# Performance work log

Hardware: AMD Instinct MI355X
Metric: run time of the kernel (lower is better)

Reference implementation:

```python
import jax, jax.numpy as jnp
import numpy as np

EPS_BN = 1e-5


def _square_distance(a, b):
    # a: [B,N,3], b: [B,S,3] -> [B,N,S]
    return (jnp.sum(a * a, -1)[:, :, None]
            - 2.0 * jnp.einsum('bnc,bsc->bns', a, b)
            + jnp.sum(b * b, -1)[:, None, :])


def _bn_relu(x, gamma, beta):
    # x: [B,C,N]; training-mode batch norm over (B,N) per channel
    mean = jnp.mean(x, axis=(0, 2), keepdims=True)
    var = jnp.var(x, axis=(0, 2), keepdims=True)
    y = (x - mean) * jax.lax.rsqrt(var + EPS_BN)
    y = y * gamma[None, :, None] + beta[None, :, None]
    return jax.nn.relu(y)


def setup_inputs() -> dict:
    key = jax.random.key(0)
    ks = jax.random.split(key, 8)
    B, N, S, D1, D2 = 16, 4096, 1024, 128, 256
    Cin, C0, C1 = D1 + D2, 256, 128
    inp = {
        'xyz1': jax.random.normal(ks[0], (B, 3, N), jnp.float32),
        'xyz2': jax.random.normal(ks[1], (B, 3, S), jnp.float32),
        'points1': jax.random.normal(ks[2], (B, D1, N), jnp.float32),
        'points2': jax.random.normal(ks[3], (B, D2, S), jnp.float32),
        # pointwise Conv1d weights (kernel size 1) as [out,in]
        'w0': jax.random.normal(ks[4], (C0, Cin), jnp.float32) * (1.0 / np.sqrt(Cin)),
        'b0': jnp.zeros((C0,), jnp.float32),
        'g0': jnp.ones((C0,), jnp.float32),
        'be0': jnp.zeros((C0,), jnp.float32),
        'w1': jax.random.normal(ks[5], (C1, C0), jnp.float32) * (1.0 / np.sqrt(C0)),
        'b1': jnp.zeros((C1,), jnp.float32),
        'g1': jnp.ones((C1,), jnp.float32),
        'be1': jnp.zeros((C1,), jnp.float32),
    }
    return inp


def reference(xyz1, xyz2, points1, points2, w0, b0, g0, be0, w1, b1, g1, be1):
    # permute to [B,N,3] / [B,S,3] / [B,S,D2]
    x1 = jnp.transpose(xyz1, (0, 2, 1))
    x2 = jnp.transpose(xyz2, (0, 2, 1))
    p2 = jnp.transpose(points2, (0, 2, 1))
    B, N, _ = x1.shape

    dists = _square_distance(x1, x2)            # [B,N,S]
    # NOTE: faithful to the source: idx comes from the sort, but the
    # weight distances are the FIRST 3 columns of the UNsorted dists
    # (the repo assigns sorted values to `dicts`, not `dists`).
    idx = jnp.argsort(dists, axis=-1)[:, :, :3]  # [B,N,3]
    d3 = jnp.maximum(dists[:, :, :3], 1e-10)     # [B,N,3]
    weight = 1.0 / d3
    weight = weight / jnp.sum(weight, axis=-1, keepdims=True)

    gathered = jax.vmap(lambda p, i: p[i])(p2, idx)          # [B,N,3,D2]
    interpolated = jnp.sum(gathered * weight[..., None], axis=2)  # [B,N,D2]

    p1 = jnp.transpose(points1, (0, 2, 1))       # [B,N,D1]
    new_points = jnp.concatenate([p1, interpolated], axis=-1)  # [B,N,Cin]
    new_points = jnp.transpose(new_points, (0, 2, 1))           # [B,Cin,N]

    h = jnp.einsum('oc,bcn->bon', w0, new_points) + b0[None, :, None]
    h = _bn_relu(h, g0, be0)
    h = jnp.einsum('oc,bcn->bon', w1, h) + b1[None, :, None]
    h = _bn_relu(h, g1, be1)
    return h
```

## Files before the change

kernel.cpp:

```cpp
#include <hip/hip_runtime.h>
#include <cstdint>
#include <cstddef>

#define BB   16
#define NN   4096
#define SS   1024
#define D1   128
#define D2   256
#define CIN  384
#define C0   256
#define C1   128
#define MM   (BB*NN)
#define NBLK (MM/128)

typedef __attribute__((ext_vector_type(8))) short short8;
typedef __attribute__((ext_vector_type(4))) float f32x4;

__device__ __forceinline__ float b2f(unsigned short h) {
    union { unsigned int u; float f; } x; x.u = ((unsigned int)h) << 16; return x.f;
}
__device__ __forceinline__ unsigned short f2b(float f) {
    union { float f; unsigned int u; } x; x.f = f;
    unsigned int r = x.u + 0x7FFFu + ((x.u >> 16) & 1u);
    return (unsigned short)(r >> 16);
}

#define GLD16(g, l) __builtin_amdgcn_global_load_lds( \
    (const __attribute__((address_space(1))) void*)(g), \
    (__attribute__((address_space(3))) void*)(l), 16, 0, 0)


#define UPD6(dd, ss, D0, D1v, D2v, J0, J1, J2) do { \
    bool ca = (dd) < D0, cb = (dd) < D1v, cc = (dd) < D2v; \
    float m1 = __builtin_amdgcn_fmed3f((dd), D0, D1v); \
    float m2 = __builtin_amdgcn_fmed3f((dd), D1v, D2v); \
    int u1 = ca ? J0 : (ss); \
    int u2 = cb ? J1 : (ss); \
    D0 = fminf((dd), D0); \
    J2 = cc ? u2 : J2; \
    J1 = cb ? u1 : J1; \
    J0 = ca ? (ss) : J0; \
    D1v = m1; D2v = m2; \
} while (0)

#define LTE(x, xj, y, yj) ((x) < (y) || ((x) == (y) && (xj) < (yj)))

__device__ __forceinline__ void knn_body(const float* __restrict__ xyz1,
                                         const float* __restrict__ xyz2,
                                         int* __restrict__ idxb, float* __restrict__ wtb,
                                         int rb, int t, char* smem)
{
    float* sx = (float*)smem;
    float* sy = sx + 8 * 132;
    float* sz = sy + 8 * 132;
    const int b = rb >> 7;
    const int bx = rb & 127;
    const int chunk = t & 7;
    const int n = bx * 32 + (t >> 3);

    for (int i = t; i < SS; i += 256) {
        int li = (i >> 7) * 132 + (i & 127);
        sx[li] = xyz2[((size_t)b * 3 + 0) * SS + i];
        sy[li] = xyz2[((size_t)b * 3 + 1) * SS + i];
        sz[li] = xyz2[((size_t)b * 3 + 2) * SS + i];
    }
    __syncthreads();

    const float px = xyz1[((size_t)b * 3 + 0) * NN + n];
    const float py = xyz1[((size_t)b * 3 + 1) * NN + n];
    const float pz = xyz1[((size_t)b * 3 + 2) * NN + n];

    float aD0 = 3.4e38f, aD1 = 3.4e38f, aD2 = 3.4e38f;
    int   aJ0 = 0, aJ1 = 0, aJ2 = 0;
    float bD0 = 3.4e38f, bD1 = 3.4e38f, bD2 = 3.4e38f;
    int   bJ0 = 0, bJ1 = 0, bJ2 = 0;

    const float* cx = sx + chunk * 132;
    const float* cy = sy + chunk * 132;
    const float* cz = sz + chunk * 132;
    const int sbase = chunk * 128;
#pragma unroll 4
    for (int s4 = 0; s4 < 32; ++s4) {
        float4 xs = *(const float4*)(cx + s4 * 4);
        float4 ys = *(const float4*)(cy + s4 * 4);
        float4 zs = *(const float4*)(cz + s4 * 4);
        int s = sbase + s4 * 4;
        { float dx=px-xs.x, dy=py-ys.x, dz=pz-zs.x; float d=dx*dx+dy*dy+dz*dz; UPD6(d, s+0, aD0,aD1,aD2,aJ0,aJ1,aJ2); }
        { float dx=px-xs.y, dy=py-ys.y, dz=pz-zs.y; float d=dx*dx+dy*dy+dz*dz; UPD6(d, s+1, bD0,bD1,bD2,bJ0,bJ1,bJ2); }
        { float dx=px-xs.z, dy=py-ys.z, dz=pz-zs.z; float d=dx*dx+dy*dy+dz*dz; UPD6(d, s+2, aD0,aD1,aD2,aJ0,aJ1,aJ2); }
        { float dx=px-xs.w, dy=py-ys.w, dz=pz-zs.w; float d=dx*dx+dy*dy+dz*dz; UPD6(d, s+3, bD0,bD1,bD2,bJ0,bJ1,bJ2); }
    }

    float d0v, d1v, d2v; int j0, j1, j2;
    {
        bool c0 = LTE(aD0, aJ0, bD0, bJ0);
        d0v = c0 ? aD0 : bD0;  j0 = c0 ? aJ0 : bJ0;
        float na0 = c0 ? aD1 : aD0, na1 = c0 ? aD2 : aD1;
        int   nx0 = c0 ? aJ1 : aJ0, nx1 = c0 ? aJ2 : aJ1;
        float nb0 = c0 ? bD0 : bD1, nb1 = c0 ? bD1 : bD2;
        int   ny0 = c0 ? bJ0 : bJ1, ny1 = c0 ? bJ1 : bJ2;
        bool c1 = LTE(na0, nx0, nb0, ny0);
        d1v = c1 ? na0 : nb0;  j1 = c1 ? nx0 : ny0;
        float ma0 = c1 ? na1 : na0;  int mx0 = c1 ? nx1 : nx0;
        float mb0 = c1 ? nb0 : nb1;  int my0 = c1 ? ny0 : ny1;
        bool c2 = LTE(ma0, mx0, mb0, my0);
        d2v = c2 ? ma0 : mb0;  j2 = c2 ? mx0 : my0;
    }

#pragma unroll
    for (int r = 1; r <= 4; r <<= 1) {
        float e0 = __shfl_xor(d0v, r), e1 = __shfl_xor(d1v, r), e2 = __shfl_xor(d2v, r);
        int   k0 = __shfl_xor(j0, r),  k1 = __shfl_xor(j1, r),  k2 = __shfl_xor(j2, r);
        bool ownlow = ((t & r) == 0);
        float a0 = ownlow ? d0v : e0, a1 = ownlow ? d1v : e1, a2 = ownlow ? d2v : e2;
        int   x0 = ownlow ? j0 : k0,  x1 = ownlow ? j1 : k1,  x2 = ownlow ? j2 : k2;
        float b0 = ownlow ? e0 : d0v, b1 = ownlow ? e1 : d1v, b2 = ownlow ? e2 : d2v;
        int   y0 = ownlow ? k0 : j0,  y1 = ownlow ? k1 : j1,  y2 = ownlow ? k2 : j2;
        bool c0 = a0 <= b0;
        d0v = c0 ? a0 : b0;  j0 = c0 ? x0 : y0;
        float na0 = c0 ? a1 : a0, na1 = c0 ? a2 : a1;
        int   nx0 = c0 ? x1 : x0, nx1 = c0 ? x2 : x1;
        float nb0 = c0 ? b0 : b1, nb1 = c0 ? b1 : b2;
        int   ny0 = c0 ? y0 : y1, ny1 = c0 ? y1 : y2;
        bool c1 = na0 <= nb0;
        d1v = c1 ? na0 : nb0;  j1 = c1 ? nx0 : ny0;
        float ma0 = c1 ? na1 : na0;  int mx0 = c1 ? nx1 : nx0;
        float mb0 = c1 ? nb0 : nb1;  int my0 = c1 ? ny0 : ny1;
        bool c2 = ma0 <= mb0;
        d2v = c2 ? ma0 : mb0;  j2 = c2 ? mx0 : my0;
    }

    if (chunk == 0) {
        float dd[3];
#pragma unroll
        for (int k = 0; k < 3; ++k) {
            float dx = px - sx[k], dy = py - sy[k], dz = pz - sz[k];
            float d = dx*dx + dy*dy + dz*dz;
            dd[k] = fmaxf(d, 1e-10f);
        }
        float r0 = 1.f/dd[0], r1 = 1.f/dd[1], r2 = 1.f/dd[2];
        float inv = 1.f / (r0 + r1 + r2);
        size_t base = ((size_t)b * NN + n) * 3;
        idxb[base+0] = j0; idxb[base+1] = j1; idxb[base+2] = j2;
        wtb[base+0] = r0*inv; wtb[base+1] = r1*inv; wtb[base+2] = r2*inv;
    }
}

__device__ __forceinline__ void transpose_body(const float* __restrict__ src,
                                               unsigned short* __restrict__ dst,
                                               int C, int Np, int dstStride,
                                               int b, int cblk, int nblk, int t, char* smem)
{
    float (*tile)[65] = (float(*)[65])smem;
    const int c0 = cblk * 64, n0 = nblk * 64;
    const int j = t & 63, i4 = t >> 6;
#pragma unroll
    for (int p = 0; p < 64; p += 4) {
        int ci = p + i4;
        tile[ci][j] = src[((size_t)b * C + c0 + ci) * Np + n0 + j];
    }
    __syncthreads();
#pragma unroll
    for (int p = 0; p < 64; p += 4) {
        int ni = p + i4;
        dst[((size_t)b * Np + n0 + ni) * dstStride + c0 + j] = f2b(tile[j][ni]);
    }
}

__global__ __launch_bounds__(256) void mega_front_k(
    const float* __restrict__ xyz1, const float* __restrict__ xyz2,
    const float* __restrict__ points1, const float* __restrict__ points2,
    const float* __restrict__ w0, const float* __restrict__ w1,
    unsigned short* __restrict__ P1T, unsigned short* __restrict__ P2T,
    unsigned short* __restrict__ w0b, unsigned short* __restrict__ w1b,
    int* __restrict__ idxb, float* __restrict__ wtb)
{
    __shared__ __align__(16) char smem[16640];
    const unsigned bid = blockIdx.x;
    const int g = bid / 86, r = bid % 86;
    const int t = threadIdx.x;

    if (r < 32) {
        knn_body(xyz1, xyz2, idxb, wtb, g * 32 + r, t, smem);
    } else if (r < 64) {
        int rb = g * 32 + (r - 32);
        transpose_body(points1, P1T, D1, NN, D1,
                       rb >> 7, (rb >> 6) & 1, rb & 63, t, smem);
    } else if (r < 80) {
        int rb = g * 16 + (r - 64);
        transpose_body(points2, P2T, D2, SS, D2,
                       rb >> 6, (rb >> 4) & 3, rb & 15, t, smem);
    } else {
        int rb = g * 6 + (r - 80);
        int i = rb * 256 + t;
        if (i < C0 * CIN) w0b[i] = f2b(w0[i]);
        if (i < C1 * C0)  w1b[i] = f2b(w1[i]);
    }
}

__launch_bounds__(512, 1)
__global__ void gemm1_k(const unsigned short* __restrict__ P1T,
                        const unsigned short* __restrict__ P2T,
                        const int* __restrict__ idxb, const float* __restrict__ wtb,
                        const unsigned short* __restrict__ w0b,
                        unsigned short* __restrict__ h1, float* __restrict__ part1)
{
    __shared__ unsigned short Als[128 * 64];
    __shared__ unsigned short Bls[256 * 64];
    __shared__ float lsum[2][256];
    __shared__ float lsq[2][256];

    const int t = threadIdx.x;
    const int wv = t >> 6, l = t & 63, g = l >> 4, lc = l & 15;
    const int wm = wv >> 2, wn = wv & 3;
    const int m0 = blockIdx.x * 128;
    const int b  = blockIdx.x >> 5;
    const int sub = t & 7;

    const int grow = t >> 2;
    const size_t gb = ((size_t)(m0 + grow)) * 3;
    const int gi0 = idxb[gb], gi1 = idxb[gb+1], gi2 = idxb[gb+2];
    const float gw0 = wtb[gb], gw1 = wtb[gb+1], gw2 = wtb[gb+2];
    const char* gp0 = (const char*)(P2T + ((size_t)b * SS + gi0) * D2) + (t & 3) * 32;
    const char* gp1 = (const char*)(P2T + ((size_t)b * SS + gi1) * D2) + (t & 3) * 32;
    const char* gp2 = (const char*)(P2T + ((size_t)b * SS + gi2) * D2) + (t & 3) * 32;
    char* gdst = (char*)Als + grow * 128;
    const int gsw = (grow & 7) << 4;

    f32x4 acc[4][4];
#pragma unroll
    for (int i = 0; i < 4; ++i)
#pragma unroll
        for (int j = 0; j < 4; ++j) acc[i][j] = (f32x4){0.f, 0.f, 0.f, 0.f};

    for (int ks = 0; ks < 6; ++ks) {
        const int k0 = ks * 64;
        __syncthreads();
        if (ks < 2) {
#pragma unroll
            for (int q = 0; q < 2; ++q) {
                int row = q * 64 + (t >> 3);
                int bco = (sub * 16) ^ ((row & 7) << 4);
                const char* src = (const char*)P1T + (((size_t)(m0 + row)) * D1 + k0) * 2 + bco;
                char* dst = (char*)Als + (q * 512 + wv * 64) * 16;
                GLD16(src, dst);
            }
        } else {
            const int cgB = (ks - 2) * 128;
#pragma unroll
            for (int h = 0; h < 2; ++h) {
                union { uint4 v; unsigned short s[8]; } a0, a1, a2, ov;
                a0.v = *(const uint4*)(gp0 + cgB + h * 16);
                a1.v = *(const uint4*)(gp1 + cgB + h * 16);
                a2.v = *(const uint4*)(gp2 + cgB + h * 16);
#pragma unroll
                for (int i = 0; i < 8; ++i)
                    ov.s[i] = f2b(gw0 * b2f(a0.s[i]) + gw1 * b2f(a1.s[i]) + gw2 * b2f(a2.s[i]));
                *(uint4*)(gdst + (((t & 3) * 32 + h * 16) ^ gsw)) = ov.v;
            }
        }
#pragma unroll
        for (int q = 0; q < 4; ++q) {
            int o = q * 64 + (t >> 3);
            int bco = (sub * 16) ^ ((o & 7) << 4);
            const char* src = (const char*)w0b + (((size_t)o) * CIN + k0) * 2 + bco;
            char* dst = (char*)Bls + (q * 512 + wv * 64) * 16;
            GLD16(src, dst);
        }
        __syncthreads();
#pragma unroll
        for (int kk = 0; kk < 2; ++kk) {
            short8 af[4], bfr[4];
#pragma unroll
            for (int fm = 0; fm < 4; ++fm) {
                int row = wm * 64 + fm * 16 + lc;
                int bcol = kk * 64 + g * 16;
                af[fm] = *(const short8*)((const char*)Als + row * 128 + (bcol ^ ((row & 7) << 4)));
            }
#pragma unroll
            for (int fn = 0; fn < 4; ++fn) {
                int o = wn * 64 + fn * 16 + lc;
                int bcol = kk * 64 + g * 16;
                bfr[fn] = *(const short8*)((const char*)Bls + o * 128 + (bcol ^ ((o & 7) << 4)));
            }
#pragma unroll
            for (int fm = 0; fm < 4; ++fm)
#pragma unroll
                for (int fn = 0; fn < 4; ++fn)
                    acc[fm][fn] = __builtin_amdgcn_mfma_f32_16x16x32_bf16(af[fm], bfr[fn], acc[fm][fn], 0, 0, 0);
        }
    }

    float s1[4] = {0,0,0,0}, s2v[4] = {0,0,0,0};
#pragma unroll
    for (int fm = 0; fm < 4; ++fm)
#pragma unroll
        for (int fn = 0; fn < 4; ++fn) {
            int row = m0 + wm * 64 + fm * 16 + g * 4;
            int col = wn * 64 + fn * 16 + lc;
#pragma unroll
            for (int j = 0; j < 4; ++j) {
                float v = acc[fm][fn][j];
                h1[((size_t)(row + j)) * C0 + col] = f2b(v);
                s1[fn] += v; s2v[fn] += v * v;
            }
        }
#pragma unroll
    for (int fn = 0; fn < 4; ++fn) {
        s1[fn] += __shfl_xor(s1[fn], 16); s1[fn] += __shfl_xor(s1[fn], 32);
        s2v[fn] += __shfl_xor(s2v[fn], 16); s2v[fn] += __shfl_xor(s2v[fn], 32);
    }
    if (l < 16) {
#pragma unroll
        for (int fn = 0; fn < 4; ++fn) {
            lsum[wm][wn * 64 + fn * 16 + l] = s1[fn];
            lsq[wm][wn * 64 + fn * 16 + l] = s2v[fn];
        }
    }
    __syncthreads();
    if (t < 256) {
        part1[(size_t)t * NBLK + blockIdx.x]        = lsum[0][t] + lsum[1][t];
        part1[(size_t)(C0 + t) * NBLK + blockIdx.x] = lsq[0][t] + lsq[1][t];
    }
}

__global__ void stats_k(const float* __restrict__ part, int nblk, int C,
                        const float* __restrict__ gam, const float* __restrict__ bet,
                        float* __restrict__ sc, float* __restrict__ sh)
{
    const int w = threadIdx.x >> 6, l = threadIdx.x & 63;
    const int o = blockIdx.x * 4 + w;
    if (o >= C) return;
    float s = 0.f, q = 0.f;
    for (int i = l; i < nblk; i += 64) {
        s += part[(size_t)o * nblk + i];
        q += part[(size_t)(C + o) * nblk + i];
    }
#pragma unroll
    for (int r = 32; r; r >>= 1) { s += __shfl_xor(s, r); q += __shfl_xor(q, r); }
    if (l == 0) {
        const float inv = 1.0f / (float)MM;
        float mean = s * inv;
        float var = q * inv - mean * mean;
        float scale = gam[o] * rsqrtf(var + 1e-5f);
        sc[o] = scale;
        sh[o] = bet[o] - mean * scale;
    }
}

__launch_bounds__(256, 1)
__global__ void gemm2_k(const unsigned short* __restrict__ h1, const unsigned short* __restrict__ w1b,
                        const float* __restrict__ sc1, const float* __restrict__ sh1,
                        unsigned short* __restrict__ h2, float* __restrict__ part2)
{
    __shared__ unsigned short Als[128 * 64];
    __shared__ unsigned short Bls[128 * 64];
    __shared__ float scl[256], shl[256];
    __shared__ float lsum[2][128];
    __shared__ float lsq[2][128];

    const int t = threadIdx.x;
    const int wv = t >> 6, l = t & 63, g = l >> 4, lc = l & 15;
    const int wm = wv >> 1, wn = wv & 1;
    const int m0 = blockIdx.x * 128;
    const int sub = t & 7;

    scl[t] = sc1[t]; shl[t] = sh1[t];

    f32x4 acc[4][4];
#pragma unroll
    for (int i = 0; i < 4; ++i)
#pragma unroll
        for (int j = 0; j < 4; ++j) acc[i][j] = (f32x4){0.f, 0.f, 0.f, 0.f};

    for (int ks = 0; ks < 4; ++ks) {
        const int k0 = ks * 64;
        __syncthreads();
        uint4 r[4];
#pragma unroll
        for (int q = 0; q < 4; ++q) {
            int row = q * 32 + (t >> 3);
            r[q] = *(const uint4*)((const char*)h1 + (((size_t)(m0 + row)) * C0 + k0) * 2 + sub * 16);
        }
#pragma unroll
        for (int q = 0; q < 4; ++q) {
            int row = q * 32 + (t >> 3);
            union { uint4 v; unsigned short s[8]; } u, ov;
            u.v = r[q];
#pragma unroll
            for (int i = 0; i < 8; ++i) {
                int k = k0 + sub * 8 + i;
                float f = b2f(u.s[i]);
                ov.s[i] = f2b(fmaxf(0.0f, fmaf(scl[k], f, shl[k])));
            }
            *(uint4*)((char*)Als + row * 128 + ((sub * 16) ^ ((row & 7) << 4))) = ov.v;
        }
#pragma unroll
        for (int q = 0; q < 4; ++q) {
            int o = q * 32 + (t >> 3);
            int bco = (sub * 16) ^ ((o & 7) << 4);
            const char* src = (const char*)w1b + (((size_t)o) * C0 + k0) * 2 + bco;
            char* dst = (char*)Bls + (q * 256 + wv * 64) * 16;
            GLD16(src, dst);
        }
        __syncthreads();
#pragma unroll
        for (int kk = 0; kk < 2; ++kk) {
            short8 af[4], bfr[4];
#pragma unroll
            for (int fm = 0; fm < 4; ++fm) {
                int row = wm * 64 + fm * 16 + lc;
                int bcol = kk * 64 + g * 16;
                af[fm] = *(const short8*)((const char*)Als + row * 128 + (bcol ^ ((row & 7) << 4)));
            }
#pragma unroll
            for (int fn = 0; fn < 4; ++fn) {
                int o = wn * 64 + fn * 16 + lc;
                int bcol = kk * 64 + g * 16;
                bfr[fn] = *(const short8*)((const char*)Bls + o * 128 + (bcol ^ ((o & 7) << 4)));
            }
#pragma unroll
            for (int fm = 0; fm < 4; ++fm)
#pragma unroll
                for (int fn = 0; fn < 4; ++fn)
                    acc[fm][fn] = __builtin_amdgcn_mfma_f32_16x16x32_bf16(af[fm], bfr[fn], acc[fm][fn], 0, 0, 0);
        }
    }

    float s1[4] = {0,0,0,0}, s2v[4] = {0,0,0,0};
#pragma unroll
    for (int fm = 0; fm < 4; ++fm)
#pragma unroll
        for (int fn = 0; fn < 4; ++fn) {
            int row = m0 + wm * 64 + fm * 16 + g * 4;
            int col = wn * 64 + fn * 16 + lc;
#pragma unroll
            for (int j = 0; j < 4; ++j) {
                float v = acc[fm][fn][j];
                h2[((size_t)(row + j)) * C1 + col] = f2b(v);
                s1[fn] += v; s2v[fn] += v * v;
            }
        }
#pragma unroll
    for (int fn = 0; fn < 4; ++fn) {
        s1[fn] += __shfl_xor(s1[fn], 16); s1[fn] += __shfl_xor(s1[fn], 32);
        s2v[fn] += __shfl_xor(s2v[fn], 16); s2v[fn] += __shfl_xor(s2v[fn], 32);
    }
    if (l < 16) {
#pragma unroll
        for (int fn = 0; fn < 4; ++fn) {
            lsum[wm][wn * 64 + fn * 16 + l] = s1[fn];
            lsq[wm][wn * 64 + fn * 16 + l] = s2v[fn];
        }
    }
    __syncthreads();
    if (t < 128) {
        part2[(size_t)t * NBLK + blockIdx.x]        = lsum[0][t] + lsum[1][t];
        part2[(size_t)(C1 + t) * NBLK + blockIdx.x] = lsq[0][t] + lsq[1][t];
    }
}

__global__ void finalize_k(const unsigned short* __restrict__ h2,
                           const float* __restrict__ sc, const float* __restrict__ sh,
                           float* __restrict__ out)
{
    __shared__ float tile[64][65];
    const int b = blockIdx.z, o0 = blockIdx.y * 64, n0 = blockIdx.x * 64;
    const int t = threadIdx.x, j = t & 63, i4 = t >> 6;
    const float scv = sc[o0 + j], shv = sh[o0 + j];
#pragma unroll
    for (int p = 0; p < 64; p += 4) {
        int ni = p + i4;
        float f = b2f(h2[((size_t)b * NN + n0 + ni) * C1 + o0 + j]);
        tile[ni][j] = fmaxf(0.0f, fmaf(scv, f, shv));
    }
    __syncthreads();
#pragma unroll
    for (int p = 0; p < 64; p += 4) {
        int oi = p + i4;
        out[((size_t)(b * C1 + o0 + oi)) * NN + n0 + j] = tile[j][oi];
    }
}

extern "C" void kernel_launch(void* const* d_in, const int* in_sizes, int n_in,
                              void* d_out, int out_size, void* d_ws, size_t ws_size,
                              hipStream_t stream)
{
    const float* xyz1    = (const float*)d_in[0];
    const float* xyz2    = (const float*)d_in[1];
    const float* points1 = (const float*)d_in[2];
    const float* points2 = (const float*)d_in[3];
    const float* w0      = (const float*)d_in[4];
    const float* g0      = (const float*)d_in[6];
    const float* be0     = (const float*)d_in[7];
    const float* w1      = (const float*)d_in[8];
    const float* g1      = (const float*)d_in[10];
    const float* be1     = (const float*)d_in[11];
    float* out = (float*)d_out;
    char* ws = (char*)d_ws;

    unsigned short* P1T = (unsigned short*)(ws + 0);
    unsigned short* h1  = (unsigned short*)(ws + 16777216);
    unsigned short* P2T = (unsigned short*)(ws + 50331648);
    unsigned short* h2  = (unsigned short*)(ws + 58720256);
    int*   idxb  = (int*)  (ws + 75497472);
    float* wtb   = (float*)(ws + 76283904);
    unsigned short* w0b = (unsigned short*)(ws + 77070336);
    unsigned short* w1b = (unsigned short*)(ws + 77266944);
    float* part1 = (float*)(ws + 77332480);
    float* part2 = (float*)(ws + 78381056);
    float* sc1   = (float*)(ws + 78905344);
    float* sh1   = (float*)(ws + 78906368);
    float* sc2   = (float*)(ws + 78907392);
    float* sh2   = (float*)(ws + 78908416);

    mega_front_k<<<86 * 64, 256, 0, stream>>>(xyz1, xyz2, points1, points2, w0, w1,
                                              P1T, P2T, w0b, w1b, idxb, wtb);
    gemm1_k<<<MM/128, 512, 0, stream>>>(P1T, P2T, idxb, wtb, w0b, h1, part1);
    stats_k<<<C0/4, 256, 0, stream>>>(part1, NBLK, C0, g0, be0, sc1, sh1);
    gemm2_k<<<MM/128, 256, 0, stream>>>(h1, w1b, sc1, sh1, h2, part2);
    stats_k<<<C1/4, 256, 0, stream>>>(part2, NBLK, C1, g1, be1, sc2, sh2);
    finalize_k<<<dim3(NN/64, C1/64, BB), 256, 0, stream>>>(h2, sc2, sh2, out);
}
```

Before: 117.4 us.

## Rewrite KNN top-3 with packed double keys and wave-split merge

Replaces the KNN top-3 selection with packed 64-bit keys (float distance in the high word, index in the low word), so min/max on doubles keep distance and index together and a sorting network replaces the compare/select chains. Each block now handles 64 query points with four waves, each scanning a quarter of the candidates straight from global memory, then merges through LDS. This drops the xyz2 LDS staging and the shuffle reduction, and halves the KNN block count, so the mega-kernel grid shrinks. The risk is FP64 min/max throughput and uncached-looking global loads replacing LDS reads. Tie-breaking by index is kept implicitly.

```diff
diff --git a/kernel.cpp b/kernel.cpp
--- a/kernel.cpp
+++ b/kernel.cpp
@@ -29,116 +29,88 @@
     (const __attribute__((address_space(1))) void*)(g), \
     (__attribute__((address_space(3))) void*)(l), 16, 0, 0)
 
-
-#define UPD6(dd, ss, D0, D1v, D2v, J0, J1, J2) do { \
-    bool ca = (dd) < D0, cb = (dd) < D1v, cc = (dd) < D2v; \
-    float m1 = __builtin_amdgcn_fmed3f((dd), D0, D1v); \
-    float m2 = __builtin_amdgcn_fmed3f((dd), D1v, D2v); \
-    int u1 = ca ? J0 : (ss); \
-    int u2 = cb ? J1 : (ss); \
-    D0 = fminf((dd), D0); \
-    J2 = cc ? u2 : J2; \
-    J1 = cb ? u1 : J1; \
-    J0 = ca ? (ss) : J0; \
-    D1v = m1; D2v = m2; \
-} while (0)
-
-#define LTE(x, xj, y, yj) ((x) < (y) || ((x) == (y) && (xj) < (yj)))
-
-__device__ __forceinline__ void knn_body(const float* __restrict__ xyz1,
-                                         const float* __restrict__ xyz2,
-                                         int* __restrict__ idxb, float* __restrict__ wtb,
-                                         int rb, int t, char* smem)
-{
-    float* sx = (float*)smem;
-    float* sy = sx + 8 * 132;
-    float* sz = sy + 8 * 132;
-    const int b = rb >> 7;
-    const int bx = rb & 127;
-    const int chunk = t & 7;
-    const int n = bx * 32 + (t >> 3);
-
-    for (int i = t; i < SS; i += 256) {
-        int li = (i >> 7) * 132 + (i & 127);
-        sx[li] = xyz2[((size_t)b * 3 + 0) * SS + i];
-        sy[li] = xyz2[((size_t)b * 3 + 1) * SS + i];
-        sz[li] = xyz2[((size_t)b * 3 + 2) * SS + i];
-    }
-    __syncthreads();
+__device__ __forceinline__ void knn_body3(const float* __restrict__ xyz1,
+                                          const float* __restrict__ xyz2,
+                                          int* __restrict__ idxb, float* __restrict__ wtb,
+                                          int rb, int t, char* smem)
+{
+    double* mrg = (double*)smem;
+    const int b    = rb >> 6;
+    const int lane = t & 63;
+    const int n    = (rb & 63) * 64 + lane;
+    const int wu   = __builtin_amdgcn_readfirstlane(t >> 6);
+
+    const float* qx = xyz2 + ((size_t)b * 3 + 0) * SS + wu * 256;
+    const float* qy = xyz2 + ((size_t)b * 3 + 1) * SS + wu * 256;
+    const float* qz = xyz2 + ((size_t)b * 3 + 2) * SS + wu * 256;
 
     const float px = xyz1[((size_t)b * 3 + 0) * NN + n];
     const float py = xyz1[((size_t)b * 3 + 1) * NN + n];
     const float pz = xyz1[((size_t)b * 3 + 2) * NN + n];
 
-    float aD0 = 3.4e38f, aD1 = 3.4e38f, aD2 = 3.4e38f;
-    int   aJ0 = 0, aJ1 = 0, aJ2 = 0;
-    float bD0 = 3.4e38f, bD1 = 3.4e38f, bD2 = 3.4e38f;
-    int   bJ0 = 0, bJ1 = 0, bJ2 = 0;
-
-    const float* cx = sx + chunk * 132;
-    const float* cy = sy + chunk * 132;
-    const float* cz = sz + chunk * 132;
-    const int sbase = chunk * 128;
+    const double INITK = __hiloint2double(0x7F7FFFFF, 0);
+    double A0 = INITK, A1 = INITK, A2 = INITK;
+    double B0 = INITK, B1 = INITK, B2 = INITK;
+    const int sb = wu * 256;
+
 #pragma unroll 4
-    for (int s4 = 0; s4 < 32; ++s4) {
-        float4 xs = *(const float4*)(cx + s4 * 4);
-        float4 ys = *(const float4*)(cy + s4 * 4);
-        float4 zs = *(const float4*)(cz + s4 * 4);
-        int s = sbase + s4 * 4;
-        { float dx=px-xs.x, dy=py-ys.x, dz=pz-zs.x; float d=dx*dx+dy*dy+dz*dz; UPD6(d, s+0, aD0,aD1,aD2,aJ0,aJ1,aJ2); }
-        { float dx=px-xs.y, dy=py-ys.y, dz=pz-zs.y; float d=dx*dx+dy*dy+dz*dz; UPD6(d, s+1, bD0,bD1,bD2,bJ0,bJ1,bJ2); }
-        { float dx=px-xs.z, dy=py-ys.z, dz=pz-zs.z; float d=dx*dx+dy*dy+dz*dz; UPD6(d, s+2, aD0,aD1,aD2,aJ0,aJ1,aJ2); }
-        { float dx=px-xs.w, dy=py-ys.w, dz=pz-zs.w; float d=dx*dx+dy*dy+dz*dz; UPD6(d, s+3, bD0,bD1,bD2,bJ0,bJ1,bJ2); }
-    }
-
-    float d0v, d1v, d2v; int j0, j1, j2;
+    for (int s = 0; s < 256; s += 2) {
+        {
+            float qxv = qx[s], qyv = qy[s], qzv = qz[s];
+            float dx = px - qxv, dy = py - qyv, dz = pz - qzv;
+            float d = dx*dx + dy*dy + dz*dz;
+            double k = __hiloint2double(__float_as_int(d), sb + s);
+            double t0 = fmin(k, A0), h0 = fmax(k, A0);
+            double t1 = fmin(h0, A1), h1 = fmax(h0, A1);
+            A2 = fmin(h1, A2); A0 = t0; A1 = t1;
+        }
+        {
+            float qxv = qx[s+1], qyv = qy[s+1], qzv = qz[s+1];
+            float dx = px - qxv, dy = py - qyv, dz = pz - qzv;
+            float d = dx*dx + dy*dy + dz*dz;
+            double k = __hiloint2double(__float_as_int(d), sb + s + 1);
+            double t0 = fmin(k, B0), h0 = fmax(k, B0);
+            double t1 = fmin(h0, B1), h1 = fmax(h0, B1);
+            B2 = fmin(h1, B2); B0 = t0; B1 = t1;
+        }
+    }
+    double K0, K1, K2;
     {
-        bool c0 = LTE(aD0, aJ0, bD0, bJ0);
-        d0v = c0 ? aD0 : bD0;  j0 = c0 ? aJ0 : bJ0;
-        float na0 = c0 ? aD1 : aD0, na1 = c0 ? aD2 : aD1;
-        int   nx0 = c0 ? aJ1 : aJ0, nx1 = c0 ? aJ2 : aJ1;
-        float nb0 = c0 ? bD0 : bD1, nb1 = c0 ? bD1 : bD2;
-        int   ny0 = c0 ? bJ0 : bJ1, ny1 = c0 ? bJ1 : bJ2;
-        bool c1 = LTE(na0, nx0, nb0, ny0);
-        d1v = c1 ? na0 : nb0;  j1 = c1 ? nx0 : ny0;
-        float ma0 = c1 ? na1 : na0;  int mx0 = c1 ? nx1 : nx0;
-        float mb0 = c1 ? nb0 : nb1;  int my0 = c1 ? ny0 : ny1;
-        bool c2 = LTE(ma0, mx0, mb0, my0);
-        d2v = c2 ? ma0 : mb0;  j2 = c2 ? mx0 : my0;
-    }
-
-#pragma unroll
-    for (int r = 1; r <= 4; r <<= 1) {
-        float e0 = __shfl_xor(d0v, r), e1 = __shfl_xor(d1v, r), e2 = __shfl_xor(d2v, r);
-        int   k0 = __shfl_xor(j0, r),  k1 = __shfl_xor(j1, r),  k2 = __shfl_xor(j2, r);
-        bool ownlow = ((t & r) == 0);
-        float a0 = ownlow ? d0v : e0, a1 = ownlow ? d1v : e1, a2 = ownlow ? d2v : e2;
-        int   x0 = ownlow ? j0 : k0,  x1 = ownlow ? j1 : k1,  x2 = ownlow ? j2 : k2;
-        float b0 = ownlow ? e0 : d0v, b1 = ownlow ? e1 : d1v, b2 = ownlow ? e2 : d2v;
-        int   y0 = ownlow ? k0 : j0,  y1 = ownlow ? k1 : j1,  y2 = ownlow ? k2 : j2;
-        bool c0 = a0 <= b0;
-        d0v = c0 ? a0 : b0;  j0 = c0 ? x0 : y0;
-        float na0 = c0 ? a1 : a0, na1 = c0 ? a2 : a1;
-        int   nx0 = c0 ? x1 : x0, nx1 = c0 ? x2 : x1;
-        float nb0 = c0 ? b0 : b1, nb1 = c0 ? b1 : b2;
-        int   ny0 = c0 ? y0 : y1, ny1 = c0 ? y1 : y2;
-        bool c1 = na0 <= nb0;
-        d1v = c1 ? na0 : nb0;  j1 = c1 ? nx0 : ny0;
-        float ma0 = c1 ? na1 : na0;  int mx0 = c1 ? nx1 : nx0;
-        float mb0 = c1 ? nb0 : nb1;  int my0 = c1 ? ny0 : ny1;
-        bool c2 = ma0 <= mb0;
-        d2v = c2 ? ma0 : mb0;  j2 = c2 ? mx0 : my0;
-    }
-
-    if (chunk == 0) {
-        float dd[3];
-#pragma unroll
-        for (int k = 0; k < 3; ++k) {
-            float dx = px - sx[k], dy = py - sy[k], dz = pz - sz[k];
-            float d = dx*dx + dy*dy + dz*dz;
-            dd[k] = fmaxf(d, 1e-10f);
-        }
-        float r0 = 1.f/dd[0], r1 = 1.f/dd[1], r2 = 1.f/dd[2];
+        double y0 = fmax(A0, B0);
+        K0 = fmin(A0, B0);
+        double x1 = fmin(A1, B1);
+        K1 = fmin(y0, x1);
+        double z  = fmax(y0, x1);
+        double x2 = fmin(A2, B2);
+        K2 = fmin(z, x2);
+    }
+    if (wu > 0) {
+        mrg[(wu * 64 + lane) * 3 + 0] = K0;
+        mrg[(wu * 64 + lane) * 3 + 1] = K1;
+        mrg[(wu * 64 + lane) * 3 + 2] = K2;
+    }
+    __syncthreads();
+    if (wu == 0) {
+#pragma unroll
+        for (int q = 1; q < 4; ++q) {
+            double C0d = mrg[(q * 64 + lane) * 3 + 0];
+            double C1d = mrg[(q * 64 + lane) * 3 + 1];
+            double C2d = mrg[(q * 64 + lane) * 3 + 2];
+            double y0 = fmax(K0, C0d);
+            K0 = fmin(K0, C0d);
+            double x1 = fmin(K1, C1d);
+            double nK1 = fmin(y0, x1);
+            double z  = fmax(y0, x1);
+            double x2 = fmin(K2, C2d);
+            K2 = fmin(z, x2);
+            K1 = nK1;
+        }
+        int j0 = __double2loint(K0), j1 = __double2loint(K1), j2 = __double2loint(K2);
+        float dd0, dd1, dd2;
+        { float dx=px-qx[0], dy=py-qy[0], dz=pz-qz[0]; dd0 = fmaxf(dx*dx+dy*dy+dz*dz, 1e-10f); }
+        { float dx=px-qx[1], dy=py-qy[1], dz=pz-qz[1]; dd1 = fmaxf(dx*dx+dy*dy+dz*dz, 1e-10f); }
+        { float dx=px-qx[2], dy=py-qy[2], dz=pz-qz[2]; dd2 = fmaxf(dx*dx+dy*dy+dz*dz, 1e-10f); }
+        float r0 = 1.f/dd0, r1 = 1.f/dd1, r2 = 1.f/dd2;
         float inv = 1.f / (r0 + r1 + r2);
         size_t base = ((size_t)b * NN + n) * 3;
         idxb[base+0] = j0; idxb[base+1] = j1; idxb[base+2] = j2;
@@ -177,21 +149,21 @@
 {
     __shared__ __align__(16) char smem[16640];
     const unsigned bid = blockIdx.x;
-    const int g = bid / 86, r = bid % 86;
+    const int g = bid / 70, r = bid % 70;
     const int t = threadIdx.x;
 
-    if (r < 32) {
-        knn_body(xyz1, xyz2, idxb, wtb, g * 32 + r, t, smem);
-    } else if (r < 64) {
-        int rb = g * 32 + (r - 32);
+    if (r < 16) {
+        knn_body3(xyz1, xyz2, idxb, wtb, g * 16 + r, t, smem);
+    } else if (r < 48) {
+        int rb = g * 32 + (r - 16);
         transpose_body(points1, P1T, D1, NN, D1,
                        rb >> 7, (rb >> 6) & 1, rb & 63, t, smem);
-    } else if (r < 80) {
-        int rb = g * 16 + (r - 64);
+    } else if (r < 64) {
+        int rb = g * 16 + (r - 48);
         transpose_body(points2, P2T, D2, SS, D2,
                        rb >> 6, (rb >> 4) & 3, rb & 15, t, smem);
     } else {
-        int rb = g * 6 + (r - 80);
+        int rb = g * 6 + (r - 64);
         int i = rb * 256 + t;
         if (i < C0 * CIN) w0b[i] = f2b(w0[i]);
         if (i < C1 * C0)  w1b[i] = f2b(w1[i]);
@@ -514,7 +486,7 @@
     float* sc2   = (float*)(ws + 78907392);
     float* sh2   = (float*)(ws + 78908416);
 
-    mega_front_k<<<86 * 64, 256, 0, stream>>>(xyz1, xyz2, points1, points2, w0, w1,
+    mega_front_k<<<70 * 64, 256, 0, stream>>>(xyz1, xyz2, points1, points2, w0, w1,
                                               P1T, P2T, w0b, w1b, idxb, wtb);
     gemm1_k<<<MM/128, 512, 0, stream>>>(P1T, P2T, idxb, wtb, w0b, h1, part1);
     stats_k<<<C0/4, 256, 0, stream>>>(part1, NBLK, C0, g0, be0, sc1, sh1);
```

Result: no change. 117.3 us (-0.1%).
